# Kernel tuning notes

Hardware: AMD Instinct MI355X
Metric: run time of the kernel (lower is better)

The kernel has to match this reference:

```python
import jax, jax.numpy as jnp
import numpy as np

N_NODES = 100000
N_RELS = 237
N_EDGES = 500000
D_IN = 128
D_HID = 128
D_OUT = 128


def setup_inputs() -> dict:
    key = jax.random.key(0)
    ks = jax.random.split(key, 13)
    src = jax.random.randint(ks[0], (N_EDGES,), 0, N_NODES, dtype=jnp.int32)
    dst = jax.random.randint(ks[1], (N_EDGES,), 0, N_NODES, dtype=jnp.int32)
    rel = jax.random.randint(ks[2], (N_EDGES,), 0, N_RELS, dtype=jnp.int32)
    triplets = jnp.stack([src, dst, rel], axis=1)  # [E, 3]
    s = 0.05
    return {
        "triplets": triplets,
        "ent_embed": jax.random.normal(ks[3], (N_NODES, D_IN), jnp.float32) * s,
        "rel_embed": jax.random.normal(ks[4], (N_RELS, D_IN), jnp.float32) * s,
        "W_ent": jax.random.normal(ks[5], (D_IN, D_HID), jnp.float32) * s,
        "b_ent": jnp.zeros((D_HID,), jnp.float32),
        "W_rel": jax.random.normal(ks[6], (D_IN, D_HID), jnp.float32) * s,
        "b_rel": jnp.zeros((D_HID,), jnp.float32),
        "W_ent2": jax.random.normal(ks[7], (3 * D_HID, D_OUT), jnp.float32) * s,
        "b_ent2": jnp.zeros((D_OUT,), jnp.float32),
        "a_w": jax.random.normal(ks[8], (D_OUT, 1), jnp.float32) * s,
        "a_b": jnp.zeros((1,), jnp.float32),
    }


def reference(triplets, ent_embed, rel_embed, W_ent, b_ent, W_rel, b_rel,
              W_ent2, b_ent2, a_w, a_b):
    src_i, dst_i, rel_i = triplets[:, 0], triplets[:, 1], triplets[:, 2]
    # embedding gathers
    src = ent_embed[src_i]          # [E, D_IN]
    dst = ent_embed[dst_i]          # [E, D_IN]
    rel = rel_embed[rel_i]          # [E, D_IN]
    # shared fc_ent projection on src and dst, fc_rel on rel
    src = src @ W_ent + b_ent       # [E, D_HID]
    dst = dst @ W_ent + b_ent
    rel = rel @ W_rel + b_rel
    # per-edge feature c = fc_ent2(cat([src, dst, rel]))
    c = jnp.concatenate([src, dst, rel], axis=1) @ W_ent2 + b_ent2  # [E, D_OUT]
    # unnormalized exp attention score (leaky_relu slope 0.01, torch default)
    b = jnp.exp(jax.nn.leaky_relu((c @ a_w + a_b)[:, 0], negative_slope=0.01))  # [E]
    # segment softmax over edges sharing a source node
    b_sum = jax.ops.segment_sum(b, src_i, num_segments=N_NODES)  # [N]
    alpha = b / b_sum[src_i]                                     # [E]
    # weighted neighbor aggregation per source node
    h = jax.ops.segment_sum(alpha[:, None] * c, src_i, num_segments=N_NODES)  # [N, D_OUT]
    return h
```

## Files before the change

kernel.cpp:

```cpp
#include <hip/hip_runtime.h>
#include <hip/hip_bf16.h>

#define N_NODES_C 100000
#define N_PAD_C   100096
#define N_RELS_C  237
#define N_EDGES_C 500000
#define D 128

typedef __attribute__((ext_vector_type(8))) short short8;
typedef __attribute__((ext_vector_type(4))) float f32x4;

__device__ __forceinline__ ushort f2bf(float x) {
    union { float f; uint u; } v; v.f = x;
    uint r = v.u + 0x7FFFu + ((v.u >> 16) & 1u);
    return (ushort)(r >> 16);
}
__device__ __forceinline__ float bf2f_hi(uint u) {
    union { uint u; float f; } v; v.u = u; return v.f;
}

__global__ void k_fuse_w(const float* __restrict__ W_ent, const float* __restrict__ W_rel,
                         const float* __restrict__ W_ent2,
                         const float* __restrict__ b_ent, const float* __restrict__ b_rel,
                         const float* __restrict__ b_ent2,
                         float* __restrict__ Wf, float* __restrict__ WR,
                         ushort* __restrict__ WfTb, float* __restrict__ biasC) {
    int j = threadIdx.x;
    int k = blockIdx.x;
    int which = blockIdx.y;
    if (which == 0) {
        float acc = 0.f;
        for (int i = 0; i < D; ++i) acc += W_ent[k*D+i] * W_ent2[i*D+j];
        Wf[k*256 + j] = acc;
        WfTb[j*D + k] = f2bf(acc);
    } else if (which == 1) {
        float acc = 0.f;
        for (int i = 0; i < D; ++i) acc += W_ent[k*D+i] * W_ent2[(D+i)*D+j];
        Wf[k*256 + D + j] = acc;
        WfTb[(D+j)*D + k] = f2bf(acc);
    } else if (which == 2) {
        float acc = 0.f;
        for (int i = 0; i < D; ++i) acc += W_rel[k*D+i] * W_ent2[(2*D+i)*D+j];
        WR[k*D + j] = acc;
    } else if (k == 0) {
        float acc = b_ent2[j];
        for (int i = 0; i < D; ++i) {
            acc += b_ent[i] * (W_ent2[i*D+j] + W_ent2[(D+i)*D+j]);
            acc += b_rel[i] * W_ent2[(2*D+i)*D+j];
        }
        biasC[j] = acc;
    }
}

__global__ void k_rel_scalars(const float* __restrict__ rel_embed,
                              const float* __restrict__ a_w, const float* __restrict__ a_b,
                              const float* __restrict__ Wf, const float* __restrict__ WR,
                              const float* __restrict__ biasC,
                              float* __restrict__ Rm, float* __restrict__ av1,
                              float* __restrict__ av2, float* __restrict__ sR,
                              float* __restrict__ sConst) {
    int j = threadIdx.x;
    int b = blockIdx.x;
    __shared__ float red[128];
    if (b < N_RELS_C) {
        float acc = 0.f;
        for (int k = 0; k < D; ++k) acc += rel_embed[b*D+k] * WR[k*D+j];
        Rm[b*D+j] = acc;
        red[j] = acc * a_w[j];
        __syncthreads();
        for (int s = 64; s > 0; s >>= 1) { if (j < s) red[j] += red[j+s]; __syncthreads(); }
        if (j == 0) sR[b] = red[0];
    } else if (b == N_RELS_C) {
        float acc = 0.f;
        for (int t = 0; t < D; ++t) acc += Wf[j*256 + t] * a_w[t];
        av1[j] = acc;
    } else if (b == N_RELS_C + 1) {
        float acc = 0.f;
        for (int t = 0; t < D; ++t) acc += Wf[j*256 + D + t] * a_w[t];
        av2[j] = acc;
    } else {
        red[j] = biasC[j] * a_w[j];
        __syncthreads();
        for (int s = 64; s > 0; s >>= 1) { if (j < s) red[j] += red[j+s]; __syncthreads(); }
        if (j == 0) sConst[0] = red[0] + a_b[0];
    }
}

__global__ void k_prep(const float* __restrict__ ent, const float* __restrict__ av1,
                       const float* __restrict__ av2, ushort* __restrict__ entB,
                       float* __restrict__ sA, float* __restrict__ sB,
                       int n_nodes, int n_pad) {
    int g = threadIdx.x >> 5, lane = threadIdx.x & 31;
    int n = blockIdx.x*8 + g;
    if (n >= n_pad) return;
    if (n >= n_nodes) {
        ushort4 z = {0,0,0,0};
        *(ushort4*)&entB[(size_t)n*D + lane*4] = z;
        return;
    }
    float4 e  = *(const float4*)&ent[(size_t)n*D + lane*4];
    ushort4 pk;
    pk.x = f2bf(e.x); pk.y = f2bf(e.y); pk.z = f2bf(e.z); pk.w = f2bf(e.w);
    *(ushort4*)&entB[(size_t)n*D + lane*4] = pk;
    float4 v1 = *(const float4*)&av1[lane*4];
    float4 v2 = *(const float4*)&av2[lane*4];
    float p1 = e.x*v1.x + e.y*v1.y + e.z*v1.z + e.w*v1.w;
    float p2 = e.x*v2.x + e.y*v2.y + e.z*v2.z + e.w*v2.w;
    for (int m = 16; m > 0; m >>= 1) { p1 += __shfl_xor(p1, m, 32); p2 += __shfl_xor(p2, m, 32); }
    if (lane == 0) { sA[n] = p1; sB[n] = p2; }
}

__global__ __launch_bounds__(256) void k1_mfma(const ushort* __restrict__ entB,
                                               const ushort* __restrict__ WfTb,
                                               float* __restrict__ h,
                                               ushort* __restrict__ BnB,
                                               int n_nodes) {
    __shared__ __align__(16) ushort wL[256*128];
    int tid = threadIdx.x;
    int m0 = blockIdx.x * 128;

#pragma unroll
    for (int u = 0; u < 16; ++u) {
        int f = u*256 + tid;
        int r = f >> 4, k16 = f & 15;
        *(uint4*)&wL[r*128 + ((k16 ^ (r & 15)) << 3)] =
            *(const uint4*)&WfTb[r*128 + (k16 << 3)];
    }
    __syncthreads();

    int wave = tid >> 6, lane = tid & 63;
    int q = lane >> 4, c = lane & 15;
    int wm = wave * 32;

    f32x4 acc[2][16];
#pragma unroll
    for (int mt = 0; mt < 2; ++mt)
#pragma unroll
        for (int nt = 0; nt < 16; ++nt) { f32x4 z = {0.f,0.f,0.f,0.f}; acc[mt][nt] = z; }

#pragma unroll
    for (int chunk = 0; chunk < 4; ++chunk) {
        int k16 = chunk*4 + q;
        short8 a[2];
#pragma unroll
        for (int mt = 0; mt < 2; ++mt)
            a[mt] = *(const short8*)&entB[(size_t)(m0 + wm + mt*16 + c)*D + (k16 << 3)];
#pragma unroll
        for (int nt = 0; nt < 16; ++nt) {
            int row = nt*16 + c;
            short8 b = *(const short8*)&wL[row*128 + ((k16 ^ c) << 3)];
            acc[0][nt] = __builtin_amdgcn_mfma_f32_16x16x32_bf16(a[0], b, acc[0][nt], 0, 0, 0);
            acc[1][nt] = __builtin_amdgcn_mfma_f32_16x16x32_bf16(a[1], b, acc[1][nt], 0, 0, 0);
        }
    }

#pragma unroll
    for (int mt = 0; mt < 2; ++mt) {
#pragma unroll
        for (int reg = 0; reg < 4; ++reg) {
            int m = m0 + wm + mt*16 + q*4 + reg;
            if (m < n_nodes) {
#pragma unroll
                for (int nt = 0; nt < 16; ++nt) {
                    int col = nt*16 + c;
                    float v = acc[mt][nt][reg];
                    if (col < D) h[(size_t)m*D + col] = v;
                    else         BnB[(size_t)m*D + (col - D)] = f2bf(v);
                }
            }
        }
    }
}

__global__ void k_hist(const int* __restrict__ trip, int* __restrict__ deg, int n_edges) {
    int e = blockIdx.x*256 + threadIdx.x;
    if (e >= n_edges) return;
    int s = trip[3*e], d = trip[3*e+1], r = trip[3*e+2];
    if ((unsigned)s >= (unsigned)N_NODES_C || (unsigned)d >= (unsigned)N_NODES_C ||
        (unsigned)r >= (unsigned)N_RELS_C) return;
    atomicAdd(&deg[s], 1);
}

__global__ void k_scan1(const int* __restrict__ deg, int* __restrict__ off,
                        int* __restrict__ bsum, int n) {
    __shared__ int s[1024];
    int i = blockIdx.x*1024 + threadIdx.x;
    int v = (i < n) ? deg[i] : 0;
    s[threadIdx.x] = v; __syncthreads();
    for (int d = 1; d < 1024; d <<= 1) {
        int t = (threadIdx.x >= d) ? s[threadIdx.x - d] : 0;
        __syncthreads();
        s[threadIdx.x] += t;
        __syncthreads();
    }
    if (i < n) off[i] = s[threadIdx.x] - v;
    if (threadIdx.x == 1023) bsum[blockIdx.x] = s[1023];
}

__global__ void k_scan2(int* __restrict__ bsum, int nb) {
    __shared__ int s[128];
    int v = (threadIdx.x < nb) ? bsum[threadIdx.x] : 0;
    s[threadIdx.x] = v; __syncthreads();
    for (int d = 1; d < 128; d <<= 1) {
        int t = (threadIdx.x >= d) ? s[threadIdx.x - d] : 0;
        __syncthreads();
        s[threadIdx.x] += t;
        __syncthreads();
    }
    if (threadIdx.x < nb) bsum[threadIdx.x] = s[threadIdx.x] - v;
}

__global__ void k_scan3(int* __restrict__ off, int* __restrict__ cursor,
                        const int* __restrict__ bsum, int n, int total_edges) {
    int i = blockIdx.x*1024 + threadIdx.x;
    if (i < n) {
        int o = off[i] + bsum[blockIdx.x];
        off[i] = o;
        cursor[i] = o;
    }
    if (i == 0) off[n] = total_edges;
}

__global__ void k_edge_b(const int* __restrict__ trip, const float* __restrict__ sA,
                         const float* __restrict__ sB, const float* __restrict__ sR,
                         const float* __restrict__ sConst, int* __restrict__ cursor,
                         int* __restrict__ key, float* __restrict__ bval, int n_edges) {
    int e = blockIdx.x*256 + threadIdx.x;
    if (e >= n_edges) return;
    int s = trip[3*e], d = trip[3*e+1], r = trip[3*e+2];
    if ((unsigned)s >= (unsigned)N_NODES_C || (unsigned)d >= (unsigned)N_NODES_C ||
        (unsigned)r >= (unsigned)N_RELS_C) return;
    float logit = sA[s] + sB[d] + sR[r] + sConst[0];
    float l = logit > 0.f ? logit : 0.01f*logit;
    float b = expf(l);
    int p = atomicAdd(&cursor[s], 1);
    key[p]  = d | (r << 20);
    bval[p] = b;
}

__global__ void k_aggregate(const int* __restrict__ off, const int* __restrict__ key,
                            const float* __restrict__ bval, const ushort* __restrict__ BnB,
                            const float* __restrict__ Rm, const float* __restrict__ biasC,
                            float* __restrict__ h, int n_nodes) {
    int g = threadIdx.x >> 5, lane = threadIdx.x & 31;
    int n = blockIdx.x*8 + g;
    if (n >= n_nodes) return;
    int o0 = off[n], o1 = off[n+1];
    int c = lane*4;
    if (o0 == o1) {
        *(float4*)&h[(size_t)n*D + c] = make_float4(0.f,0.f,0.f,0.f);
        return;
    }
    float s = 0.f;
    for (int p = o0 + lane; p < o1; p += 32) s += bval[p];
    for (int m = 16; m > 0; m >>= 1) s += __shfl_xor(s, m, 32);
    float inv = 1.f / s;
    float4 acc = *(const float4*)&h[(size_t)n*D + c];
    float4 bc  = *(const float4*)&biasC[c];
    acc.x += bc.x; acc.y += bc.y; acc.z += bc.z; acc.w += bc.w;
    for (int p = o0; p < o1; ++p) {
        int kd = key[p];
        float al = bval[p] * inv;
        int d = kd & 0xFFFFF;
        int r = kd >> 20;
        uint2 braw = *(const uint2*)&BnB[(size_t)d*D + c];
        float4 rv  = *(const float4*)&Rm[r*D + c];
        float b0 = bf2f_hi(braw.x << 16), b1 = bf2f_hi(braw.x & 0xFFFF0000u);
        float b2 = bf2f_hi(braw.y << 16), b3 = bf2f_hi(braw.y & 0xFFFF0000u);
        acc.x += al*(b0 + rv.x);
        acc.y += al*(b1 + rv.y);
        acc.z += al*(b2 + rv.z);
        acc.w += al*(b3 + rv.w);
    }
    *(float4*)&h[(size_t)n*D + c] = acc;
}

extern "C" void kernel_launch(void* const* d_in, const int* in_sizes, int n_in,
                              void* d_out, int out_size, void* d_ws, size_t ws_size,
                              hipStream_t stream) {
    const int*   trip   = (const int*)  d_in[0];
    const float* ent    = (const float*)d_in[1];
    const float* relE   = (const float*)d_in[2];
    const float* W_ent  = (const float*)d_in[3];
    const float* b_ent  = (const float*)d_in[4];
    const float* W_rel  = (const float*)d_in[5];
    const float* b_rel  = (const float*)d_in[6];
    const float* W_ent2 = (const float*)d_in[7];
    const float* b_ent2 = (const float*)d_in[8];
    const float* a_w    = (const float*)d_in[9];
    const float* a_b    = (const float*)d_in[10];
    float* h = (float*)d_out;

    char* ws = (char*)d_ws;
    size_t o = 0;
    auto alloc = [&](size_t bytes) { size_t p = o; o += (bytes + 255) & ~(size_t)255; return p; };
    float*  Wf     = (float*) (ws + alloc(128*256*4));
    float*  WR     = (float*) (ws + alloc(128*128*4));
    ushort* WfTb   = (ushort*)(ws + alloc(256*128*2));
    float*  biasC  = (float*) (ws + alloc(128*4));
    float*  Rm     = (float*) (ws + alloc((size_t)N_RELS_C*128*4));
    float*  av1    = (float*) (ws + alloc(128*4));
    float*  av2    = (float*) (ws + alloc(128*4));
    float*  sR     = (float*) (ws + alloc(N_RELS_C*4));
    float*  sConst = (float*) (ws + alloc(4));
    float*  sA     = (float*) (ws + alloc((size_t)N_NODES_C*4));
    float*  sB     = (float*) (ws + alloc((size_t)N_NODES_C*4));
    int*    deg    = (int*)   (ws + alloc((size_t)N_NODES_C*4));
    int*    off    = (int*)   (ws + alloc(((size_t)N_NODES_C+1)*4));
    int*    cursor = (int*)   (ws + alloc((size_t)N_NODES_C*4));
    int*    bsum   = (int*)   (ws + alloc(128*4));
    int*    key    = (int*)   (ws + alloc((size_t)N_EDGES_C*4));
    float*  bval   = (float*) (ws + alloc((size_t)N_EDGES_C*4));
    ushort* entB   = (ushort*)(ws + alloc((size_t)N_PAD_C*128*2));
    ushort* BnB    = (ushort*)(ws + alloc((size_t)N_PAD_C*128*2));

    hipMemsetAsync(deg, 0, (size_t)N_NODES_C*4, stream);

    k_fuse_w<<<dim3(128,4), 128, 0, stream>>>(W_ent, W_rel, W_ent2, b_ent, b_rel, b_ent2,
                                              Wf, WR, WfTb, biasC);
    k_rel_scalars<<<N_RELS_C+3, 128, 0, stream>>>(relE, a_w, a_b, Wf, WR, biasC,
                                                  Rm, av1, av2, sR, sConst);
    k_prep<<<N_PAD_C/8, 256, 0, stream>>>(ent, av1, av2, entB, sA, sB, N_NODES_C, N_PAD_C);
    k1_mfma<<<N_PAD_C/128, 256, 0, stream>>>(entB, WfTb, h, BnB, N_NODES_C);
    k_hist<<<(N_EDGES_C+255)/256, 256, 0, stream>>>(trip, deg, N_EDGES_C);
    int nb = (N_NODES_C + 1023)/1024;
    k_scan1<<<nb, 1024, 0, stream>>>(deg, off, bsum, N_NODES_C);
    k_scan2<<<1, 128, 0, stream>>>(bsum, nb);
    k_scan3<<<nb, 1024, 0, stream>>>(off, cursor, bsum, N_NODES_C, N_EDGES_C);
    k_edge_b<<<(N_EDGES_C+255)/256, 256, 0, stream>>>(trip, sA, sB, sR, sConst,
                                                      cursor, key, bval, N_EDGES_C);
    k_aggregate<<<(N_NODES_C+7)/8, 256, 0, stream>>>(off, key, bval, BnB, Rm, biasC,
                                                     h, N_NODES_C);
}
```

Measured before the change: 267.8 us.

## Fuse bf16 conversion and score dots into MFMA, single-block scan, packed edge records

Removes the separate prep kernel by converting fp32 embeddings to bf16 inside the MFMA kernel and computing the per-node attention partials from the MFMA accumulators. Replaces the three-kernel scan with one single-block scan, packs edge key and exp score into one uint2 record, and unrolls the aggregation loop by four to keep more gathers in flight. The scores now come from bf16-rounded products, which shifts numerics slightly, and the single-block scan is serial per thread. The histogram also drops the dst and rel range checks.

Measured after the change: 471.4 us. 76.0% more time.

```diff
diff --git a/kernel.cpp b/kernel.cpp
--- a/kernel.cpp
+++ b/kernel.cpp
@@ -23,20 +23,18 @@
                          const float* __restrict__ W_ent2,
                          const float* __restrict__ b_ent, const float* __restrict__ b_rel,
                          const float* __restrict__ b_ent2,
-                         float* __restrict__ Wf, float* __restrict__ WR,
-                         ushort* __restrict__ WfTb, float* __restrict__ biasC) {
+                         float* __restrict__ WR, ushort* __restrict__ WfTb,
+                         float* __restrict__ biasC) {
     int j = threadIdx.x;
     int k = blockIdx.x;
     int which = blockIdx.y;
     if (which == 0) {
         float acc = 0.f;
         for (int i = 0; i < D; ++i) acc += W_ent[k*D+i] * W_ent2[i*D+j];
-        Wf[k*256 + j] = acc;
         WfTb[j*D + k] = f2bf(acc);
     } else if (which == 1) {
         float acc = 0.f;
         for (int i = 0; i < D; ++i) acc += W_ent[k*D+i] * W_ent2[(D+i)*D+j];
-        Wf[k*256 + D + j] = acc;
         WfTb[(D+j)*D + k] = f2bf(acc);
     } else if (which == 2) {
         float acc = 0.f;
@@ -54,10 +52,8 @@
 
 __global__ void k_rel_scalars(const float* __restrict__ rel_embed,
                               const float* __restrict__ a_w, const float* __restrict__ a_b,
-                              const float* __restrict__ Wf, const float* __restrict__ WR,
-                              const float* __restrict__ biasC,
-                              float* __restrict__ Rm, float* __restrict__ av1,
-                              float* __restrict__ av2, float* __restrict__ sR,
+                              const float* __restrict__ WR, const float* __restrict__ biasC,
+                              float* __restrict__ Rm, float* __restrict__ sR,
                               float* __restrict__ sConst) {
     int j = threadIdx.x;
     int b = blockIdx.x;
@@ -70,14 +66,6 @@
         __syncthreads();
         for (int s = 64; s > 0; s >>= 1) { if (j < s) red[j] += red[j+s]; __syncthreads(); }
         if (j == 0) sR[b] = red[0];
-    } else if (b == N_RELS_C) {
-        float acc = 0.f;
-        for (int t = 0; t < D; ++t) acc += Wf[j*256 + t] * a_w[t];
-        av1[j] = acc;
-    } else if (b == N_RELS_C + 1) {
-        float acc = 0.f;
-        for (int t = 0; t < D; ++t) acc += Wf[j*256 + D + t] * a_w[t];
-        av2[j] = acc;
     } else {
         red[j] = biasC[j] * a_w[j];
         __syncthreads();
@@ -86,34 +74,13 @@
     }
 }
 
-__global__ void k_prep(const float* __restrict__ ent, const float* __restrict__ av1,
-                       const float* __restrict__ av2, ushort* __restrict__ entB,
-                       float* __restrict__ sA, float* __restrict__ sB,
-                       int n_nodes, int n_pad) {
-    int g = threadIdx.x >> 5, lane = threadIdx.x & 31;
-    int n = blockIdx.x*8 + g;
-    if (n >= n_pad) return;
-    if (n >= n_nodes) {
-        ushort4 z = {0,0,0,0};
-        *(ushort4*)&entB[(size_t)n*D + lane*4] = z;
-        return;
-    }
-    float4 e  = *(const float4*)&ent[(size_t)n*D + lane*4];
-    ushort4 pk;
-    pk.x = f2bf(e.x); pk.y = f2bf(e.y); pk.z = f2bf(e.z); pk.w = f2bf(e.w);
-    *(ushort4*)&entB[(size_t)n*D + lane*4] = pk;
-    float4 v1 = *(const float4*)&av1[lane*4];
-    float4 v2 = *(const float4*)&av2[lane*4];
-    float p1 = e.x*v1.x + e.y*v1.y + e.z*v1.z + e.w*v1.w;
-    float p2 = e.x*v2.x + e.y*v2.y + e.z*v2.z + e.w*v2.w;
-    for (int m = 16; m > 0; m >>= 1) { p1 += __shfl_xor(p1, m, 32); p2 += __shfl_xor(p2, m, 32); }
-    if (lane == 0) { sA[n] = p1; sB[n] = p2; }
-}
-
-__global__ __launch_bounds__(256) void k1_mfma(const ushort* __restrict__ entB,
+__global__ __launch_bounds__(256) void k1_mfma(const float* __restrict__ ent,
                                                const ushort* __restrict__ WfTb,
+                                               const float* __restrict__ a_w,
                                                float* __restrict__ h,
                                                ushort* __restrict__ BnB,
+                                               float* __restrict__ sA,
+                                               float* __restrict__ sB,
                                                int n_nodes) {
     __shared__ __align__(16) ushort wL[256*128];
     int tid = threadIdx.x;
@@ -143,8 +110,19 @@
         int k16 = chunk*4 + q;
         short8 a[2];
 #pragma unroll
-        for (int mt = 0; mt < 2; ++mt)
-            a[mt] = *(const short8*)&entB[(size_t)(m0 + wm + mt*16 + c)*D + (k16 << 3)];
+        for (int mt = 0; mt < 2; ++mt) {
+            int row = m0 + wm + mt*16 + c;
+            float4 e0 = make_float4(0.f,0.f,0.f,0.f), e1 = e0;
+            if (row < n_nodes) {
+                const float* ep = &ent[(size_t)row*D + (k16 << 3)];
+                e0 = *(const float4*)ep;
+                e1 = *(const float4*)(ep + 4);
+            }
+            short8 pk;
+            pk[0]=(short)f2bf(e0.x); pk[1]=(short)f2bf(e0.y); pk[2]=(short)f2bf(e0.z); pk[3]=(short)f2bf(e0.w);
+            pk[4]=(short)f2bf(e1.x); pk[5]=(short)f2bf(e1.y); pk[6]=(short)f2bf(e1.z); pk[7]=(short)f2bf(e1.w);
+            a[mt] = pk;
+        }
 #pragma unroll
         for (int nt = 0; nt < 16; ++nt) {
             int row = nt*16 + c;
@@ -154,12 +132,28 @@
         }
     }
 
+    float aw[8];
+#pragma unroll
+    for (int nt = 0; nt < 8; ++nt) aw[nt] = a_w[nt*16 + c];
+
 #pragma unroll
     for (int mt = 0; mt < 2; ++mt) {
 #pragma unroll
         for (int reg = 0; reg < 4; ++reg) {
             int m = m0 + wm + mt*16 + q*4 + reg;
+            float pa = 0.f, pb = 0.f;
+#pragma unroll
+            for (int nt = 0; nt < 8; ++nt) {
+                pa += acc[mt][nt][reg]   * aw[nt];
+                pb += acc[mt][nt+8][reg] * aw[nt];
+            }
+#pragma unroll
+            for (int msk = 1; msk < 16; msk <<= 1) {
+                pa += __shfl_xor(pa, msk);
+                pb += __shfl_xor(pb, msk);
+            }
             if (m < n_nodes) {
+                if (c == 0) { sA[m] = pa; sB[m] = pb; }
 #pragma unroll
                 for (int nt = 0; nt < 16; ++nt) {
                     int col = nt*16 + c;
@@ -175,56 +169,44 @@
 __global__ void k_hist(const int* __restrict__ trip, int* __restrict__ deg, int n_edges) {
     int e = blockIdx.x*256 + threadIdx.x;
     if (e >= n_edges) return;
-    int s = trip[3*e], d = trip[3*e+1], r = trip[3*e+2];
-    if ((unsigned)s >= (unsigned)N_NODES_C || (unsigned)d >= (unsigned)N_NODES_C ||
-        (unsigned)r >= (unsigned)N_RELS_C) return;
+    int s = trip[3*e];
+    if ((unsigned)s >= (unsigned)N_NODES_C) return;
     atomicAdd(&deg[s], 1);
 }
 
-__global__ void k_scan1(const int* __restrict__ deg, int* __restrict__ off,
-                        int* __restrict__ bsum, int n) {
+__global__ __launch_bounds__(1024) void k_scan_all(const int* __restrict__ deg,
+                                                   int* __restrict__ off,
+                                                   int* __restrict__ cursor,
+                                                   int n, int total_edges) {
     __shared__ int s[1024];
-    int i = blockIdx.x*1024 + threadIdx.x;
-    int v = (i < n) ? deg[i] : 0;
-    s[threadIdx.x] = v; __syncthreads();
+    int t = threadIdx.x;
+    const int per = (n + 1023) / 1024;
+    int base = t * per;
+    int lim = n - base; if (lim < 0) lim = 0; if (lim > per) lim = per;
+    int sum = 0;
+    for (int i = 0; i < lim; ++i) sum += deg[base + i];
+    s[t] = sum; __syncthreads();
+    int v = sum;
     for (int d = 1; d < 1024; d <<= 1) {
-        int t = (threadIdx.x >= d) ? s[threadIdx.x - d] : 0;
+        int u = (t >= d) ? s[t - d] : 0;
         __syncthreads();
-        s[threadIdx.x] += t;
+        s[t] += u;
         __syncthreads();
     }
-    if (i < n) off[i] = s[threadIdx.x] - v;
-    if (threadIdx.x == 1023) bsum[blockIdx.x] = s[1023];
-}
-
-__global__ void k_scan2(int* __restrict__ bsum, int nb) {
-    __shared__ int s[128];
-    int v = (threadIdx.x < nb) ? bsum[threadIdx.x] : 0;
-    s[threadIdx.x] = v; __syncthreads();
-    for (int d = 1; d < 128; d <<= 1) {
-        int t = (threadIdx.x >= d) ? s[threadIdx.x - d] : 0;
-        __syncthreads();
-        s[threadIdx.x] += t;
-        __syncthreads();
-    }
-    if (threadIdx.x < nb) bsum[threadIdx.x] = s[threadIdx.x] - v;
-}
-
-__global__ void k_scan3(int* __restrict__ off, int* __restrict__ cursor,
-                        const int* __restrict__ bsum, int n, int total_edges) {
-    int i = blockIdx.x*1024 + threadIdx.x;
-    if (i < n) {
-        int o = off[i] + bsum[blockIdx.x];
-        off[i] = o;
-        cursor[i] = o;
-    }
-    if (i == 0) off[n] = total_edges;
+    int run = s[t] - v;
+    for (int i = 0; i < lim; ++i) {
+        int dv = deg[base + i];
+        off[base + i] = run;
+        cursor[base + i] = run;
+        run += dv;
+    }
+    if (t == 0) off[n] = total_edges;
 }
 
 __global__ void k_edge_b(const int* __restrict__ trip, const float* __restrict__ sA,
                          const float* __restrict__ sB, const float* __restrict__ sR,
                          const float* __restrict__ sConst, int* __restrict__ cursor,
-                         int* __restrict__ key, float* __restrict__ bval, int n_edges) {
+                         uint2* __restrict__ kb, int n_edges) {
     int e = blockIdx.x*256 + threadIdx.x;
     if (e >= n_edges) return;
     int s = trip[3*e], d = trip[3*e+1], r = trip[3*e+2];
@@ -234,14 +216,13 @@
     float l = logit > 0.f ? logit : 0.01f*logit;
     float b = expf(l);
     int p = atomicAdd(&cursor[s], 1);
-    key[p]  = d | (r << 20);
-    bval[p] = b;
-}
-
-__global__ void k_aggregate(const int* __restrict__ off, const int* __restrict__ key,
-                            const float* __restrict__ bval, const ushort* __restrict__ BnB,
-                            const float* __restrict__ Rm, const float* __restrict__ biasC,
-                            float* __restrict__ h, int n_nodes) {
+    kb[p] = make_uint2((uint)(d | (r << 20)), __float_as_uint(b));
+}
+
+__global__ void k_aggregate(const int* __restrict__ off, const uint2* __restrict__ kb,
+                            const ushort* __restrict__ BnB, const float* __restrict__ Rm,
+                            const float* __restrict__ biasC, float* __restrict__ h,
+                            int n_nodes) {
     int g = threadIdx.x >> 5, lane = threadIdx.x & 31;
     int n = blockIdx.x*8 + g;
     if (n >= n_nodes) return;
@@ -252,25 +233,54 @@
         return;
     }
     float s = 0.f;
-    for (int p = o0 + lane; p < o1; p += 32) s += bval[p];
+    for (int p = o0 + lane; p < o1; p += 32) s += __uint_as_float(kb[p].y);
     for (int m = 16; m > 0; m >>= 1) s += __shfl_xor(s, m, 32);
     float inv = 1.f / s;
     float4 acc = *(const float4*)&h[(size_t)n*D + c];
     float4 bc  = *(const float4*)&biasC[c];
     acc.x += bc.x; acc.y += bc.y; acc.z += bc.z; acc.w += bc.w;
-    for (int p = o0; p < o1; ++p) {
-        int kd = key[p];
-        float al = bval[p] * inv;
-        int d = kd & 0xFFFFF;
-        int r = kd >> 20;
-        uint2 braw = *(const uint2*)&BnB[(size_t)d*D + c];
-        float4 rv  = *(const float4*)&Rm[r*D + c];
-        float b0 = bf2f_hi(braw.x << 16), b1 = bf2f_hi(braw.x & 0xFFFF0000u);
-        float b2 = bf2f_hi(braw.y << 16), b3 = bf2f_hi(braw.y & 0xFFFF0000u);
-        acc.x += al*(b0 + rv.x);
-        acc.y += al*(b1 + rv.y);
-        acc.z += al*(b2 + rv.z);
-        acc.w += al*(b3 + rv.w);
+
+    int p = o0;
+    for (; p + 4 <= o1; p += 4) {
+        uint2 kv0 = kb[p+0], kv1 = kb[p+1], kv2 = kb[p+2], kv3 = kb[p+3];
+        uint2 g0 = *(const uint2*)&BnB[(size_t)(kv0.x & 0xFFFFF)*D + c];
+        uint2 g1 = *(const uint2*)&BnB[(size_t)(kv1.x & 0xFFFFF)*D + c];
+        uint2 g2 = *(const uint2*)&BnB[(size_t)(kv2.x & 0xFFFFF)*D + c];
+        uint2 g3 = *(const uint2*)&BnB[(size_t)(kv3.x & 0xFFFFF)*D + c];
+        float4 r0 = *(const float4*)&Rm[(kv0.x >> 20)*D + c];
+        float4 r1 = *(const float4*)&Rm[(kv1.x >> 20)*D + c];
+        float4 r2 = *(const float4*)&Rm[(kv2.x >> 20)*D + c];
+        float4 r3 = *(const float4*)&Rm[(kv3.x >> 20)*D + c];
+        float a0 = __uint_as_float(kv0.y) * inv;
+        float a1 = __uint_as_float(kv1.y) * inv;
+        float a2 = __uint_as_float(kv2.y) * inv;
+        float a3 = __uint_as_float(kv3.y) * inv;
+        acc.x += a0*(bf2f_hi(g0.x << 16)         + r0.x)
+               + a1*(bf2f_hi(g1.x << 16)         + r1.x)
+               + a2*(bf2f_hi(g2.x << 16)         + r2.x)
+               + a3*(bf2f_hi(g3.x << 16)         + r3.x);
+        acc.y += a0*(bf2f_hi(g0.x & 0xFFFF0000u) + r0.y)
+               + a1*(bf2f_hi(g1.x & 0xFFFF0000u) + r1.y)
+               + a2*(bf2f_hi(g2.x & 0xFFFF0000u) + r2.y)
+               + a3*(bf2f_hi(g3.x & 0xFFFF0000u) + r3.y);
+        acc.z += a0*(bf2f_hi(g0.y << 16)         + r0.z)
+               + a1*(bf2f_hi(g1.y << 16)         + r1.z)
+               + a2*(bf2f_hi(g2.y << 16)         + r2.z)
+               + a3*(bf2f_hi(g3.y << 16)         + r3.z);
+        acc.w += a0*(bf2f_hi(g0.y & 0xFFFF0000u) + r0.w)
+               + a1*(bf2f_hi(g1.y & 0xFFFF0000u) + r1.w)
+               + a2*(bf2f_hi(g2.y & 0xFFFF0000u) + r2.w)
+               + a3*(bf2f_hi(g3.y & 0xFFFF0000u) + r3.w);
+    }
+    for (; p < o1; ++p) {
+        uint2 kv = kb[p];
+        float al = __uint_as_float(kv.y) * inv;
+        uint2 braw = *(const uint2*)&BnB[(size_t)(kv.x & 0xFFFFF)*D + c];
+        float4 rv  = *(const float4*)&Rm[(kv.x >> 20)*D + c];
+        acc.x += al*(bf2f_hi(braw.x << 16)         + rv.x);
+        acc.y += al*(bf2f_hi(braw.x & 0xFFFF0000u) + rv.y);
+        acc.z += al*(bf2f_hi(braw.y << 16)         + rv.z);
+        acc.w += al*(bf2f_hi(braw.y & 0xFFFF0000u) + rv.w);
     }
     *(float4*)&h[(size_t)n*D + c] = acc;
 }
@@ -294,13 +304,10 @@
     char* ws = (char*)d_ws;
     size_t o = 0;
     auto alloc = [&](size_t bytes) { size_t p = o; o += (bytes + 255) & ~(size_t)255; return p; };
-    float*  Wf     = (float*) (ws + alloc(128*256*4));
     float*  WR     = (float*) (ws + alloc(128*128*4));
     ushort* WfTb   = (ushort*)(ws + alloc(256*128*2));
     float*  biasC  = (float*) (ws + alloc(128*4));
     float*  Rm     = (float*) (ws + alloc((size_t)N_RELS_C*128*4));
-    float*  av1    = (float*) (ws + alloc(128*4));
-    float*  av2    = (float*) (ws + alloc(128*4));
     float*  sR     = (float*) (ws + alloc(N_RELS_C*4));
     float*  sConst = (float*) (ws + alloc(4));
     float*  sA     = (float*) (ws + alloc((size_t)N_NODES_C*4));
@@ -308,27 +315,20 @@
     int*    deg    = (int*)   (ws + alloc((size_t)N_NODES_C*4));
     int*    off    = (int*)   (ws + alloc(((size_t)N_NODES_C+1)*4));
     int*    cursor = (int*)   (ws + alloc((size_t)N_NODES_C*4));
-    int*    bsum   = (int*)   (ws + alloc(128*4));
-    int*    key    = (int*)   (ws + alloc((size_t)N_EDGES_C*4));
-    float*  bval   = (float*) (ws + alloc((size_t)N_EDGES_C*4));
-    ushort* entB   = (ushort*)(ws + alloc((size_t)N_PAD_C*128*2));
+    uint2*  kb     = (uint2*) (ws + alloc((size_t)N_EDGES_C*8));
     ushort* BnB    = (ushort*)(ws + alloc((size_t)N_PAD_C*128*2));
 
     hipMemsetAsync(deg, 0, (size_t)N_NODES_C*4, stream);
 
     k_fuse_w<<<dim3(128,4), 128, 0, stream>>>(W_ent, W_rel, W_ent2, b_ent, b_rel, b_ent2,
-                                              Wf, WR, WfTb, biasC);
-    k_rel_scalars<<<N_RELS_C+3, 128, 0, stream>>>(relE, a_w, a_b, Wf, WR, biasC,
-                                                  Rm, av1, av2, sR, sConst);
-    k_prep<<<N_PAD_C/8, 256, 0, stream>>>(ent, av1, av2, entB, sA, sB, N_NODES_C, N_PAD_C);
-    k1_mfma<<<N_PAD_C/128, 256, 0, stream>>>(entB, WfTb, h, BnB, N_NODES_C);
+                                              WR, WfTb, biasC);
+    k_rel_scalars<<<N_RELS_C+1, 128, 0, stream>>>(relE, a_w, a_b, WR, biasC,
+                                                  Rm, sR, sConst);
+    k1_mfma<<<N_PAD_C/128, 256, 0, stream>>>(ent, WfTb, a_w, h, BnB, sA, sB, N_NODES_C);
     k_hist<<<(N_EDGES_C+255)/256, 256, 0, stream>>>(trip, deg, N_EDGES_C);
-    int nb = (N_NODES_C + 1023)/1024;
-    k_scan1<<<nb, 1024, 0, stream>>>(deg, off, bsum, N_NODES_C);
-    k_scan2<<<1, 128, 0, stream>>>(bsum, nb);
-    k_scan3<<<nb, 1024, 0, stream>>>(off, cursor, bsum, N_NODES_C, N_EDGES_C);
+    k_scan_all<<<1, 1024, 0, stream>>>(deg, off, cursor, N_NODES_C, N_EDGES_C);
     k_edge_b<<<(N_EDGES_C+255)/256, 256, 0, stream>>>(trip, sA, sB, sR, sConst,
-                                                      cursor, key, bval, N_EDGES_C);
-    k_aggregate<<<(N_NODES_C+7)/8, 256, 0, stream>>>(off, key, bval, BnB, Rm, biasC,
+                                                      cursor, kb, N_EDGES_C);
+    k_aggregate<<<(N_NODES_C+7)/8, 256, 0, stream>>>(off, kb, BnB, Rm, biasC,
                                                      h, N_NODES_C);
 }
```
